# Optimization experiments

Hardware: AMD Instinct MI355X
Metric: run time of the kernel (lower is better)

Reference implementation:

```python
import jax, jax.numpy as jnp
import numpy as np

# Dimensions (match init_kwargs): input_dim=512, slot_size=512 -> k_dim=256, v_dim=512
B, T, D = 32, 128, 512        # batch, seq_len, input_dim
KD, VD = 256, 512             # k_dim = slot_size//2, v_dim = slot_size
S = 4                         # binding_num_slots (flag='binding')
NK = 16384                    # n_keys
K = 32                        # top_k


def setup_inputs() -> dict:
    key = jax.random.key(0)
    ks = jax.random.split(key, 7)
    kb = 1.0 / np.sqrt(KD)
    return {
        "x": jax.random.normal(ks[0], (B, T, D), jnp.float32),
        # query_proj: Linear(input_dim -> k_dim)
        "Wq": jax.random.normal(ks[1], (D, KD), jnp.float32) * (1.0 / np.sqrt(D)),
        "bq": jnp.zeros((KD,), jnp.float32),
        # per-slot keys (uniform +-1/sqrt(k_dim) as in get_uniform_keys)
        "keys": jax.random.uniform(ks[2], (S, NK, KD), jnp.float32, minval=-kb, maxval=kb),
        # per-slot EmbeddingBag value tables, N(0, v_dim^-0.5)
        "values": jax.random.normal(ks[3], (S, NK, VD), jnp.float32) * (VD ** -0.5),
        # residual_linear: Linear(k_dim -> v_dim)
        "Wr": jax.random.normal(ks[4], (KD, VD), jnp.float32) * (1.0 / np.sqrt(KD)),
        "br": jnp.zeros((VD,), jnp.float32),
    }


def reference(x, Wq, bq, keys, values, Wr, br):
    # flag='binding'; dropout is eval-mode (identity).
    bs = B * T
    q = x.reshape(bs, D) @ Wq + bq                      # (bs, KD)
    # normalize keys per key vector, then score all slots at once
    kn = keys / jnp.linalg.norm(keys, axis=-1, keepdims=True)  # (S, NK, KD)
    scores = jnp.einsum('bk,snk->sbn', q, kn)           # (S, bs, NK)
    top_s, top_i = jax.lax.top_k(scores, K)             # (S, bs, K)
    w = jax.nn.softmax(top_s, axis=-1)                  # softmax over top-k scores
    # EmbeddingBag(mode='sum', per_sample_weights): gather then weighted sum
    gathered = jax.vmap(lambda v, i: v[i])(values, top_i)      # (S, bs, K, VD)
    out = jnp.einsum('sbk,sbkv->sbv', w, gathered)      # (S, bs, VD)
    out = out.transpose(1, 0, 2)                        # (bs, S, VD)
    out = out + (q @ Wr + br)[:, None, :]               # residual (broadcast over slots)
    return out.reshape(B, T, S, VD)
```

## Files before the change

### kernel.cpp

```cpp
#include <hip/hip_runtime.h>

typedef unsigned short u16;
typedef unsigned int   u32;
typedef __attribute__((ext_vector_type(8))) short  short8;
typedef __attribute__((ext_vector_type(8))) u16    ushort8;
typedef __attribute__((ext_vector_type(4))) u16    ushort4v;
typedef __attribute__((ext_vector_type(4))) float  f32x4;

#define AS1 __attribute__((address_space(1)))
#define AS3 __attribute__((address_space(3)))

#define CSTRIDE 16
#define CAPB 20

__device__ __forceinline__ float bf2f(u16 u) {
    union { u32 i; float f; } x; x.i = ((u32)u) << 16; return x.f;
}
__device__ __forceinline__ u16 f2bf(float f) {
    union { float f; u32 i; } x; x.f = f;
    u32 r = x.i + 0x7fffu + ((x.i >> 16) & 1u);
    return (u16)(r >> 16);
}


__global__ __launch_bounds__(256) void k_transpose_cast(
    const float* __restrict__ src, u16* __restrict__ dst, int R, int C)
{
    int i = blockIdx.x * 256 + threadIdx.x;
    if (i >= R * C) return;
    int r = i / C, c = i - r * C;
    dst[(size_t)c * R + r] = f2bf(src[i]);
}

__global__ __launch_bounds__(256) void k_cast8(
    const float* __restrict__ src, u16* __restrict__ dst)
{
    size_t i = ((size_t)blockIdx.x * 256 + threadIdx.x) * 8;
    float4 a = *(const float4*)(src + i);
    float4 b = *(const float4*)(src + i + 4);
    ushort8 o;
    o[0] = f2bf(a.x); o[1] = f2bf(a.y); o[2] = f2bf(a.z); o[3] = f2bf(a.w);
    o[4] = f2bf(b.x); o[5] = f2bf(b.y); o[6] = f2bf(b.z); o[7] = f2bf(b.w);
    *(ushort8*)(dst + i) = o;
}

__global__ __launch_bounds__(256) void k_norm_keys(
    const float* __restrict__ keys, u16* __restrict__ kn)
{
    int key  = blockIdx.x * 4 + (threadIdx.x >> 6);
    int lane = threadIdx.x & 63;
    const float* kp = keys + (size_t)key * 256 + lane * 4;
    float4 v = *(const float4*)kp;
    float ss = v.x * v.x + v.y * v.y + v.z * v.z + v.w * v.w;
#pragma unroll
    for (int o = 32; o; o >>= 1) ss += __shfl_xor(ss, o);
    float sc = 1.0f / sqrtf(ss);
    ushort4v o4;
    o4[0] = f2bf(v.x * sc); o4[1] = f2bf(v.y * sc);
    o4[2] = f2bf(v.z * sc); o4[3] = f2bf(v.w * sc);
    *(ushort4v*)(kn + (size_t)key * 256 + lane * 4) = o4;
}

__global__ __launch_bounds__(256) void k_rownorm(
    const u16* __restrict__ q, float* __restrict__ rn)
{
    int row  = blockIdx.x * 4 + (threadIdx.x >> 6);
    int lane = threadIdx.x & 63;
    ushort4v u = *(const ushort4v*)(q + (size_t)row * 256 + lane * 4);
    float a = bf2f(u[0]), b = bf2f(u[1]), c = bf2f(u[2]), d = bf2f(u[3]);
    float ss = a * a + b * b + c * c + d * d;
#pragma unroll
    for (int o = 32; o; o >>= 1) ss += __shfl_xor(ss, o);
    if (lane == 0) rn[row] = sqrtf(ss);
}

template<int EPI>
__global__ __launch_bounds__(256) void gemm_nt(
    const short* __restrict__ A, const short* __restrict__ B,
    void* __restrict__ Cp, const float* __restrict__ bias,
    int M, int N, int K, int ldc)
{
    __shared__ __align__(16) short lA[128 * 32];
    __shared__ __align__(16) short lB[128 * 32];
    const int t  = threadIdx.x;
    const int m0 = blockIdx.y << 7, n0 = blockIdx.x << 7;
    const int w  = t >> 6, lane = t & 63;
    const int wr = (w >> 1) << 6, wc = (w & 1) << 6;
    const int qr = lane & 15, qh = lane >> 4;

    f32x4 acc[4][4];
#pragma unroll
    for (int i = 0; i < 4; ++i)
#pragma unroll
        for (int j = 0; j < 4; ++j) acc[i][j] = (f32x4){0.f, 0.f, 0.f, 0.f};

    const short* ga0 = A + (size_t)(m0 + (t >> 2)) * K + (t & 3) * 8;
    const short* ga1 = ga0 + (size_t)64 * K;
    const short* gb0 = B + (size_t)(n0 + (t >> 2)) * K + (t & 3) * 8;
    const short* gb1 = gb0 + (size_t)64 * K;
    char* lAb = (char*)lA + w * 1024;
    char* lBb = (char*)lB + w * 1024;

    for (int k0 = 0; k0 < K; k0 += 32) {
        __builtin_amdgcn_global_load_lds((const AS1 void*)(ga0 + k0), (AS3 void*)lAb,          16, 0, 0);
        __builtin_amdgcn_global_load_lds((const AS1 void*)(ga1 + k0), (AS3 void*)(lAb + 4096), 16, 0, 0);
        __builtin_amdgcn_global_load_lds((const AS1 void*)(gb0 + k0), (AS3 void*)lBb,          16, 0, 0);
        __builtin_amdgcn_global_load_lds((const AS1 void*)(gb1 + k0), (AS3 void*)(lBb + 4096), 16, 0, 0);
        __syncthreads();
        short8 af[4], bfr[4];
#pragma unroll
        for (int i = 0; i < 4; ++i) af[i]  = *(const short8*)&lA[(wr + i * 16 + qr) * 32 + qh * 8];
#pragma unroll
        for (int i = 0; i < 4; ++i) bfr[i] = *(const short8*)&lB[(wc + i * 16 + qr) * 32 + qh * 8];
#pragma unroll
        for (int mi = 0; mi < 4; ++mi)
#pragma unroll
            for (int ni = 0; ni < 4; ++ni)
                acc[mi][ni] = __builtin_amdgcn_mfma_f32_16x16x32_bf16(af[mi], bfr[ni], acc[mi][ni], 0, 0, 0);
        __syncthreads();
    }

#pragma unroll
    for (int mi = 0; mi < 4; ++mi)
#pragma unroll
        for (int ni = 0; ni < 4; ++ni) {
            const int col = n0 + wc + ni * 16 + qr;
            float bv = bias[col];
            f32x4 a = acc[mi][ni];
#pragma unroll
            for (int j = 0; j < 4; ++j) {
                const int row = m0 + wr + mi * 16 + qh * 4 + j;
                float v = a[j] + bv;
                if (EPI == 2) ((float*)Cp)[(size_t)row * ldc + col] = v;
                else          ((u16*)Cp)[(size_t)row * ldc + col]  = f2bf(v);
            }
        }
}

__global__ __launch_bounds__(256) void gemm_scores(
    const short* __restrict__ A, const short* __restrict__ Bk,
    const float* __restrict__ rn, u32* __restrict__ cnt,
    float2* __restrict__ cand, int cap, float cmul)
{
    __shared__ __align__(16) short lA[128 * 32];
    __shared__ __align__(16) short lB[128 * 32];
    __shared__ u32    lcnt[128];
    __shared__ float2 lbuf[128][CAPB];

    const int t  = threadIdx.x;
    const int m0 = blockIdx.y << 7, n0 = blockIdx.x << 7;
    const int w  = t >> 6, lane = t & 63;
    const int wr = (w >> 1) << 6, wc = (w & 1) << 6;
    const int qr = lane & 15, qh = lane >> 4;
    const int K  = 256;

    const short* ga0 = A + (size_t)(m0 + (t >> 2)) * K + (t & 3) * 8;
    const short* ga1 = ga0 + (size_t)64 * K;
    char* lAb = (char*)lA + w * 1024;
    char* lBb = (char*)lB + w * 1024;

    for (int s = 0; s < 4; ++s) {
        const short* gb0 = Bk + (size_t)s * 16384 * 256
                              + (size_t)(n0 + (t >> 2)) * K + (t & 3) * 8;
        const short* gb1 = gb0 + (size_t)64 * K;

        f32x4 acc[4][4];
#pragma unroll
        for (int i = 0; i < 4; ++i)
#pragma unroll
            for (int j = 0; j < 4; ++j) acc[i][j] = (f32x4){0.f, 0.f, 0.f, 0.f};

        for (int k0 = 0; k0 < K; k0 += 32) {
            __builtin_amdgcn_global_load_lds((const AS1 void*)(ga0 + k0), (AS3 void*)lAb,          16, 0, 0);
            __builtin_amdgcn_global_load_lds((const AS1 void*)(ga1 + k0), (AS3 void*)(lAb + 4096), 16, 0, 0);
            __builtin_amdgcn_global_load_lds((const AS1 void*)(gb0 + k0), (AS3 void*)lBb,          16, 0, 0);
            __builtin_amdgcn_global_load_lds((const AS1 void*)(gb1 + k0), (AS3 void*)(lBb + 4096), 16, 0, 0);
            __syncthreads();
            short8 af[4], bfr[4];
#pragma unroll
            for (int i = 0; i < 4; ++i) af[i]  = *(const short8*)&lA[(wr + i * 16 + qr) * 32 + qh * 8];
#pragma unroll
            for (int i = 0; i < 4; ++i) bfr[i] = *(const short8*)&lB[(wc + i * 16 + qr) * 32 + qh * 8];
#pragma unroll
            for (int mi = 0; mi < 4; ++mi)
#pragma unroll
                for (int ni = 0; ni < 4; ++ni)
                    acc[mi][ni] = __builtin_amdgcn_mfma_f32_16x16x32_bf16(af[mi], bfr[ni], acc[mi][ni], 0, 0, 0);
            __syncthreads();
        }

        u32*    cnts  = cnt  + (size_t)s * 4096 * CSTRIDE;
        float2* cands = cand + (size_t)s * 4096 * cap;

        if (t < 128) lcnt[t] = 0;
        __syncthreads();

#pragma unroll
        for (int mi = 0; mi < 4; ++mi) {
            const int rbase = wr + mi * 16 + qh * 4;
            float thrj[4];
#pragma unroll
            for (int j = 0; j < 4; ++j)
                thrj[j] = cmul * rn[m0 + rbase + j];
#pragma unroll
            for (int ni = 0; ni < 4; ++ni) {
                const int col = n0 + wc + ni * 16 + qr;
                f32x4 a = acc[mi][ni];
#pragma unroll
                for (int j = 0; j < 4; ++j) {
                    float v = a[j];
                    if (v > thrj[j]) {
                        const int rl = rbase + j;
                        u32 p = atomicAdd(&lcnt[rl], 1u);
                        if (p < CAPB)
                            lbuf[rl][p] = make_float2(v, __uint_as_float((u32)col));
                    }
                }
            }
        }
        __syncthreads();

        if (t < 128) {
            int c = (int)lcnt[t];
            if (c > CAPB) c = CAPB;
            if (c > 0) {
                const int row = m0 + t;
                u32 base = atomicAdd(&cnts[(size_t)row * CSTRIDE], (u32)c);
                float2* dst = cands + (size_t)row * cap;
                for (int i = 0; i < c; ++i) {
                    u32 p = base + (u32)i;
                    if (p < (u32)cap) dst[p] = lbuf[t][i];
                }
            }
        }
        __syncthreads();
    }
}

__global__ __launch_bounds__(256) void k_select(
    const u32* __restrict__ cnt, const float2* __restrict__ cand, int cap,
    const void* __restrict__ vtab,
    const float* __restrict__ res,
    float* __restrict__ out,
    int useBf)
{
    __shared__ float2 cbuf[4][512];
    __shared__ float  topw[4][32];
    __shared__ int    topi[4][32];

    const int t = threadIdx.x;
    const int w = t >> 6, lane = t & 63;
    const int wid = blockIdx.x * 4 + w;
    const int s   = wid >> 12;
    const int row = wid & 4095;
    const int g   = s * 4096 + row;

    int c = (int)cnt[(size_t)g * CSTRIDE];
    if (c > cap) c = cap;
    const float2* cp = cand + (size_t)g * cap;
    for (int i = lane; i < c; i += 64) cbuf[w][i] = cp[i];

    for (int k = 0; k < 32; ++k) {
        float bv = -3.0e38f; int bi = 0x7fffffff; int bp = -1;
        for (int i = lane; i < c; i += 64) {
            float2 e = cbuf[w][i];
            float v = e.x; int id = (int)__float_as_uint(e.y);
            if (v > bv || (v == bv && id < bi)) { bv = v; bi = id; bp = i; }
        }
#pragma unroll
        for (int o = 32; o; o >>= 1) {
            float ov = __shfl_xor(bv, o);
            int   oi = __shfl_xor(bi, o);
            int   op = __shfl_xor(bp, o);
            if (ov > bv || (ov == bv && oi < bi)) { bv = ov; bi = oi; bp = op; }
        }
        if (lane == 0) {
            topw[w][k] = bv;
            topi[w][k] = (bi == 0x7fffffff) ? 0 : bi;
            if (bp >= 0) cbuf[w][bp].x = -3.0e38f;
        }
    }

    if (lane < 32) {
        float v  = topw[w][lane];
        float mx = topw[w][0];
        float e  = expf(v - mx);
        float sum = e;
#pragma unroll
        for (int o = 16; o; o >>= 1) sum += __shfl_xor(sum, o, 32);
        topw[w][lane] = e / sum;
    }

    const int v0 = lane * 8;
    float a[8];
    {
        float4 r0v = *(const float4*)(res + (size_t)row * 512 + v0);
        float4 r1v = *(const float4*)(res + (size_t)row * 512 + v0 + 4);
        a[0] = r0v.x; a[1] = r0v.y; a[2] = r0v.z; a[3] = r0v.w;
        a[4] = r1v.x; a[5] = r1v.y; a[6] = r1v.z; a[7] = r1v.w;
    }
    if (useBf) {
        const u16* vt = (const u16*)vtab + (size_t)s * 16384 * 512;
#pragma unroll 8
        for (int k = 0; k < 32; ++k) {
            float w2 = topw[w][k];
            ushort8 u = *(const ushort8*)(vt + (size_t)topi[w][k] * 512 + v0);
#pragma unroll
            for (int i = 0; i < 8; ++i) a[i] += w2 * bf2f(u[i]);
        }
    } else {
        const float* vt = (const float*)vtab + (size_t)s * 16384 * 512;
#pragma unroll 4
        for (int k = 0; k < 32; ++k) {
            float w2 = topw[w][k];
            const float* vp = vt + (size_t)topi[w][k] * 512 + v0;
            float4 u0 = *(const float4*)vp;
            float4 u1 = *(const float4*)(vp + 4);
            a[0] += w2 * u0.x; a[1] += w2 * u0.y; a[2] += w2 * u0.z; a[3] += w2 * u0.w;
            a[4] += w2 * u1.x; a[5] += w2 * u1.y; a[6] += w2 * u1.z; a[7] += w2 * u1.w;
        }
    }
    float* op = out + ((size_t)row * 4 + s) * 512 + v0;
    *(float4*)op       = (float4){a[0], a[1], a[2], a[3]};
    *(float4*)(op + 4) = (float4){a[4], a[5], a[6], a[7]};
}


extern "C" void kernel_launch(void* const* d_in, const int* in_sizes, int n_in,
                              void* d_out, int out_size, void* d_ws, size_t ws_size,
                              hipStream_t stream)
{
    const float* x    = (const float*)d_in[0];
    const float* Wq   = (const float*)d_in[1];
    const float* bq   = (const float*)d_in[2];
    const float* keys = (const float*)d_in[3];
    const float* vals = (const float*)d_in[4];
    const float* Wr   = (const float*)d_in[5];
    const float* br   = (const float*)d_in[6];
    float* out = (float*)d_out;
    char*  ws  = (char*)d_ws;

    constexpr int BS = 4096, D = 512, KD = 256, VD = 512, S = 4, NK = 16384;

    size_t pos = 0;
    auto take = [&](size_t bytes) -> size_t {
        size_t p = (pos + 255) & ~(size_t)255; pos = p + bytes; return p;
    };
    size_t o_xbf = take((size_t)BS * D * 2);
    size_t o_wqt = take((size_t)KD * D * 2);
    size_t o_wrt = take((size_t)VD * KD * 2);
    size_t o_qbf = take((size_t)BS * KD * 2);
    size_t o_res = take((size_t)BS * VD * 4);
    size_t o_kn  = take((size_t)S * NK * KD * 2);
    size_t o_rn  = take((size_t)BS * 4);
    size_t o_cnt = take((size_t)S * BS * CSTRIDE * 4);
    size_t core_end = pos;

    const size_t vbf_b = (size_t)S * NK * VD * 2;
    auto cand_b = [&](int cap) { return (size_t)S * BS * cap * 8; };
    bool use_vbf = false; int cap = 192; float cmul = 2.45f / 16.0f;
    if (core_end + vbf_b + cand_b(512) + 1024 <= ws_size) {
        use_vbf = true;  cap = 512; cmul = 2.1f / 16.0f;
    } else if (core_end + cand_b(512) + 1024 <= ws_size) {
        use_vbf = false; cap = 512; cmul = 2.1f / 16.0f;
    } else if (core_end + cand_b(320) + 1024 <= ws_size) {
        use_vbf = false; cap = 320; cmul = 2.3f / 16.0f;
    }
    size_t o_vbf  = use_vbf ? take(vbf_b) : 0;
    size_t o_cand = take(cand_b(cap));

    hipMemsetAsync(ws + o_cnt, 0, (size_t)S * BS * CSTRIDE * 4, stream);

    k_transpose_cast<<<(D * KD + 255) / 256, 256, 0, stream>>>(Wq, (u16*)(ws + o_wqt), D, KD);
    k_transpose_cast<<<(KD * VD + 255) / 256, 256, 0, stream>>>(Wr, (u16*)(ws + o_wrt), KD, VD);
    k_cast8<<<(BS * D) / 2048, 256, 0, stream>>>(x, (u16*)(ws + o_xbf));
    if (use_vbf)
        k_cast8<<<(S * NK * VD) / 2048, 256, 0, stream>>>(vals, (u16*)(ws + o_vbf));
    k_norm_keys<<<(S * NK) / 4, 256, 0, stream>>>(keys, (u16*)(ws + o_kn));

    gemm_nt<1><<<dim3(KD / 128, BS / 128), 256, 0, stream>>>(
        (const short*)(ws + o_xbf), (const short*)(ws + o_wqt),
        ws + o_qbf, bq, BS, KD, D, KD);
    k_rownorm<<<BS / 4, 256, 0, stream>>>((const u16*)(ws + o_qbf), (float*)(ws + o_rn));
    gemm_nt<2><<<dim3(VD / 128, BS / 128), 256, 0, stream>>>(
        (const short*)(ws + o_qbf), (const short*)(ws + o_wrt),
        ws + o_res, br, BS, VD, KD, VD);

    gemm_scores<<<dim3(NK / 128, BS / 128), 256, 0, stream>>>(
        (const short*)(ws + o_qbf), (const short*)(ws + o_kn),
        (const float*)(ws + o_rn), (u32*)(ws + o_cnt),
        (float2*)(ws + o_cand), cap, cmul);

    const void* vtab = use_vbf ? (const void*)(ws + o_vbf) : (const void*)vals;
    k_select<<<(S * BS) / 4, 256, 0, stream>>>(
        (const u32*)(ws + o_cnt), (const float2*)(ws + o_cand), cap,
        vtab, (const float*)(ws + o_res), out, use_vbf ? 1 : 0);
}
```

Before: 564.2 us.

## Triple-buffer LDS tiles and flatten slot/k loops in scores GEMM

The per-slot and per-k-step loops in gemm_scores are merged into one 32-step loop. Each step's A/B tiles are prefetched two steps ahead into a three-deep LDS ring with global_load_lds, using explicit vmcnt waits and s_barrier in place of double __syncthreads per step. The goal is to hide global load latency behind MFMA work, including across slot boundaries where the candidate-filter epilogue runs. In exchange, LDS use per block rises, which may cut occupancy, and correctness depends on the hand-written waitcnt and barrier sequencing.

```diff
diff --git a/kernel.cpp b/kernel.cpp
--- a/kernel.cpp
+++ b/kernel.cpp
@@ -142,8 +142,8 @@
     const float* __restrict__ rn, u32* __restrict__ cnt,
     float2* __restrict__ cand, int cap, float cmul)
 {
-    __shared__ __align__(16) short lA[128 * 32];
-    __shared__ __align__(16) short lB[128 * 32];
+    __shared__ __align__(16) short lA3[3][128 * 32];
+    __shared__ __align__(16) short lB3[3][128 * 32];
     __shared__ u32    lcnt[128];
     __shared__ float2 lbuf[128][CAPB];
 
@@ -156,84 +156,107 @@
 
     const short* ga0 = A + (size_t)(m0 + (t >> 2)) * K + (t & 3) * 8;
     const short* ga1 = ga0 + (size_t)64 * K;
-    char* lAb = (char*)lA + w * 1024;
-    char* lBb = (char*)lB + w * 1024;
-
-    for (int s = 0; s < 4; ++s) {
-        const short* gb0 = Bk + (size_t)s * 16384 * 256
-                              + (size_t)(n0 + (t >> 2)) * K + (t & 3) * 8;
-        const short* gb1 = gb0 + (size_t)64 * K;
-
-        f32x4 acc[4][4];
-#pragma unroll
-        for (int i = 0; i < 4; ++i)
-#pragma unroll
-            for (int j = 0; j < 4; ++j) acc[i][j] = (f32x4){0.f, 0.f, 0.f, 0.f};
-
-        for (int k0 = 0; k0 < K; k0 += 32) {
-            __builtin_amdgcn_global_load_lds((const AS1 void*)(ga0 + k0), (AS3 void*)lAb,          16, 0, 0);
-            __builtin_amdgcn_global_load_lds((const AS1 void*)(ga1 + k0), (AS3 void*)(lAb + 4096), 16, 0, 0);
-            __builtin_amdgcn_global_load_lds((const AS1 void*)(gb0 + k0), (AS3 void*)lBb,          16, 0, 0);
-            __builtin_amdgcn_global_load_lds((const AS1 void*)(gb1 + k0), (AS3 void*)(lBb + 4096), 16, 0, 0);
-            __syncthreads();
-            short8 af[4], bfr[4];
-#pragma unroll
-            for (int i = 0; i < 4; ++i) af[i]  = *(const short8*)&lA[(wr + i * 16 + qr) * 32 + qh * 8];
-#pragma unroll
-            for (int i = 0; i < 4; ++i) bfr[i] = *(const short8*)&lB[(wc + i * 16 + qr) * 32 + qh * 8];
-#pragma unroll
-            for (int mi = 0; mi < 4; ++mi)
-#pragma unroll
-                for (int ni = 0; ni < 4; ++ni)
-                    acc[mi][ni] = __builtin_amdgcn_mfma_f32_16x16x32_bf16(af[mi], bfr[ni], acc[mi][ni], 0, 0, 0);
-            __syncthreads();
-        }
-
-        u32*    cnts  = cnt  + (size_t)s * 4096 * CSTRIDE;
-        float2* cands = cand + (size_t)s * 4096 * cap;
-
-        if (t < 128) lcnt[t] = 0;
-        __syncthreads();
-
-#pragma unroll
-        for (int mi = 0; mi < 4; ++mi) {
-            const int rbase = wr + mi * 16 + qh * 4;
-            float thrj[4];
-#pragma unroll
-            for (int j = 0; j < 4; ++j)
-                thrj[j] = cmul * rn[m0 + rbase + j];
-#pragma unroll
-            for (int ni = 0; ni < 4; ++ni) {
-                const int col = n0 + wc + ni * 16 + qr;
-                f32x4 a = acc[mi][ni];
-#pragma unroll
-                for (int j = 0; j < 4; ++j) {
-                    float v = a[j];
-                    if (v > thrj[j]) {
-                        const int rl = rbase + j;
-                        u32 p = atomicAdd(&lcnt[rl], 1u);
-                        if (p < CAPB)
-                            lbuf[rl][p] = make_float2(v, __uint_as_float((u32)col));
+    const short* gbb = Bk + (size_t)(n0 + (t >> 2)) * K + (t & 3) * 8;
+
+    auto STAGE = [&](int g, int b) {
+        const int k0 = (g & 7) * 32;
+        const int sl = g >> 3;
+        const short* gb0 = gbb + (size_t)sl * 16384 * 256 + k0;
+        char* la = (char*)&lA3[b][0] + w * 1024;
+        char* lb = (char*)&lB3[b][0] + w * 1024;
+        __builtin_amdgcn_global_load_lds((const AS1 void*)(ga0 + k0),        (AS3 void*)la,          16, 0, 0);
+        __builtin_amdgcn_global_load_lds((const AS1 void*)(ga1 + k0),        (AS3 void*)(la + 4096), 16, 0, 0);
+        __builtin_amdgcn_global_load_lds((const AS1 void*)gb0,               (AS3 void*)lb,          16, 0, 0);
+        __builtin_amdgcn_global_load_lds((const AS1 void*)(gb0 + 64 * 256),  (AS3 void*)(lb + 4096), 16, 0, 0);
+    };
+
+    f32x4 acc[4][4];
+#pragma unroll
+    for (int i = 0; i < 4; ++i)
+#pragma unroll
+        for (int j = 0; j < 4; ++j) acc[i][j] = (f32x4){0.f, 0.f, 0.f, 0.f};
+
+    STAGE(0, 0);
+    STAGE(1, 1);
+    asm volatile("s_waitcnt vmcnt(4)" ::: "memory");
+    __builtin_amdgcn_s_barrier();
+    __builtin_amdgcn_sched_barrier(0);
+
+    for (int g = 0; g < 32; ++g) {
+        const int cur = g % 3;
+        if (g + 2 < 32) STAGE(g + 2, (g + 2) % 3);
+
+        short8 af[4], bfr[4];
+#pragma unroll
+        for (int i = 0; i < 4; ++i) af[i]  = *(const short8*)&lA3[cur][(wr + i * 16 + qr) * 32 + qh * 8];
+#pragma unroll
+        for (int i = 0; i < 4; ++i) bfr[i] = *(const short8*)&lB3[cur][(wc + i * 16 + qr) * 32 + qh * 8];
+#pragma unroll
+        for (int mi = 0; mi < 4; ++mi)
+#pragma unroll
+            for (int ni = 0; ni < 4; ++ni)
+                acc[mi][ni] = __builtin_amdgcn_mfma_f32_16x16x32_bf16(af[mi], bfr[ni], acc[mi][ni], 0, 0, 0);
+
+        if (g < 30)      asm volatile("s_waitcnt vmcnt(4)" ::: "memory");
+        else if (g == 30) asm volatile("s_waitcnt vmcnt(0)" ::: "memory");
+        __builtin_amdgcn_s_barrier();
+        __builtin_amdgcn_sched_barrier(0);
+
+        if ((g & 7) == 7) {
+            const int sl = g >> 3;
+            u32*    cnts  = cnt  + (size_t)sl * 4096 * CSTRIDE;
+            float2* cands = cand + (size_t)sl * 4096 * cap;
+
+            if (t < 128) lcnt[t] = 0;
+            asm volatile("s_waitcnt lgkmcnt(0)" ::: "memory");
+            __builtin_amdgcn_s_barrier();
+            __builtin_amdgcn_sched_barrier(0);
+
+#pragma unroll
+            for (int mi = 0; mi < 4; ++mi) {
+                const int rbase = wr + mi * 16 + qh * 4;
+                float thrj[4];
+#pragma unroll
+                for (int j = 0; j < 4; ++j)
+                    thrj[j] = cmul * rn[m0 + rbase + j];
+#pragma unroll
+                for (int ni = 0; ni < 4; ++ni) {
+                    const int col = n0 + wc + ni * 16 + qr;
+                    f32x4 a = acc[mi][ni];
+#pragma unroll
+                    for (int j = 0; j < 4; ++j) {
+                        float v = a[j];
+                        if (v > thrj[j]) {
+                            const int rl = rbase + j;
+                            u32 p = atomicAdd(&lcnt[rl], 1u);
+                            if (p < CAPB)
+                                lbuf[rl][p] = make_float2(v, __uint_as_float((u32)col));
+                        }
                     }
                 }
             }
-        }
-        __syncthreads();
-
-        if (t < 128) {
-            int c = (int)lcnt[t];
-            if (c > CAPB) c = CAPB;
-            if (c > 0) {
-                const int row = m0 + t;
-                u32 base = atomicAdd(&cnts[(size_t)row * CSTRIDE], (u32)c);
-                float2* dst = cands + (size_t)row * cap;
-                for (int i = 0; i < c; ++i) {
-                    u32 p = base + (u32)i;
-                    if (p < (u32)cap) dst[p] = lbuf[t][i];
+            asm volatile("s_waitcnt lgkmcnt(0)" ::: "memory");
+            __builtin_amdgcn_s_barrier();
+            __builtin_amdgcn_sched_barrier(0);
+
+            if (t < 128) {
+                int c = (int)lcnt[t];
+                if (c > CAPB) c = CAPB;
+                if (c > 0) {
+                    const int row = m0 + t;
+                    u32 base = atomicAdd(&cnts[(size_t)row * CSTRIDE], (u32)c);
+                    float2* dst = cands + (size_t)row * cap;
+                    for (int i = 0; i < c; ++i) {
+                        u32 p = base + (u32)i;
+                        if (p < (u32)cap) dst[p] = lbuf[t][i];
+                    }
                 }
             }
-        }
-        __syncthreads();
+#pragma unroll
+            for (int i = 0; i < 4; ++i)
+#pragma unroll
+                for (int j = 0; j < 4; ++j) acc[i][j] = (f32x4){0.f, 0.f, 0.f, 0.f};
+        }
     }
 }
 
```

Measured after the change: 680.2 us. 1.21x slower.
